# Optimization experiments

Hardware: AMD Instinct MI355X
Metric: run time of the kernel (lower is better)

The kernel has to match this reference:

```python
import jax, jax.numpy as jnp
import numpy as np

NUM_ROUTING_ITERATIONS = 3


def _squash(t, axis=-1):
    # scale * t / ||t||, scale = ||t||^2 / (1 + ||t||^2)
    squared_norm = jnp.sum(t * t, axis=axis, keepdims=True)
    return squared_norm / (1.0 + squared_norm) * t / jnp.sqrt(squared_norm)


def setup_inputs() -> dict:
    key = jax.random.key(0)
    k_x, k_w = jax.random.split(key)
    B, R, C, O, I = 64, 2048, 16, 32, 16
    x = jax.random.normal(k_x, (B, R, I), dtype=jnp.float32)
    W = jax.random.normal(k_w, (R, C, O, I), dtype=jnp.float32)
    return {"x": x, "W": W}


def reference(x, W):
    # u_hat[b,r,c,o] = sum_i W[r,c,o,i] * x[b,r,i]
    u_hat = jnp.einsum('rcoi,bri->brco', W, x)  # [B,R,C,O]
    B, R, C, O = u_hat.shape
    b = jnp.zeros((B, R, C), dtype=u_hat.dtype)  # routing logits
    v = None
    for _ in range(NUM_ROUTING_ITERATIONS):
        c = jax.nn.softmax(b, axis=2)                      # softmax over capsules (dim=2)
        s = jnp.einsum('brc,brco->bro', c, u_hat)          # (c * u_hat).sum(dim=2)
        v = _squash(s, axis=-1)                            # [B,R,O]
        b = b + jnp.einsum('brco,bro->brc', u_hat, v)      # agreement update
    return v
```

## Files before the change

kernel.cpp:

```cpp
#include <hip/hip_runtime.h>

#define R_DIM 2048
#define O_DIM 32
#define I_DIM 16
#define B_DIM 64
#define BB 16

typedef _Float16 half4  __attribute__((ext_vector_type(4)));
typedef float    f32x4  __attribute__((ext_vector_type(4)));

struct SplitH4 { half4 h1, h2; };

__device__ __forceinline__ SplitH4 splitf16x4(const float* __restrict__ p) {
    const float4 f = *(const float4*)p;
    const auto a0 = __builtin_amdgcn_cvt_pkrtz(f.x, f.y);
    const auto a1 = __builtin_amdgcn_cvt_pkrtz(f.z, f.w);
    const auto c0 = __builtin_amdgcn_cvt_pkrtz(f.x - (float)a0[0], f.y - (float)a0[1]);
    const auto c1 = __builtin_amdgcn_cvt_pkrtz(f.z - (float)a1[0], f.w - (float)a1[1]);
    SplitH4 s;
    s.h1[0] = (_Float16)a0[0]; s.h1[1] = (_Float16)a0[1];
    s.h1[2] = (_Float16)a1[0]; s.h1[3] = (_Float16)a1[1];
    s.h2[0] = (_Float16)c0[0]; s.h2[1] = (_Float16)c0[1];
    s.h2[2] = (_Float16)c1[0]; s.h2[3] = (_Float16)c1[1];
    return s;
}

template<int CTRL>
__device__ __forceinline__ float dpp_mv(float v) {
    int t = __builtin_amdgcn_update_dpp(0, __float_as_int(v), CTRL, 0xf, 0xf, true);
    return __int_as_float(t);
}
__device__ __forceinline__ float row16_sum(float v) {
    v += dpp_mv<0xB1>(v);
    v += dpp_mv<0x4E>(v);
    v += dpp_mv<0x124>(v);
    v += dpp_mv<0x128>(v);
    return v;
}
__device__ __forceinline__ float row16_max(float v) {
    v = fmaxf(v, dpp_mv<0xB1>(v));
    v = fmaxf(v, dpp_mv<0x4E>(v));
    v = fmaxf(v, dpp_mv<0x124>(v));
    v = fmaxf(v, dpp_mv<0x128>(v));
    return v;
}
__device__ __forceinline__ float ror1(float v) { return dpp_mv<0x121>(v); }
__device__ __forceinline__ float ror2(float v) { return dpp_mv<0x122>(v); }

__global__ __launch_bounds__(512, 8)
void capsule_routing_kernel(const float* __restrict__ x,
                            const float* __restrict__ W,
                            float* __restrict__ out) {
    __shared__ float u_lds[BB * 512];

    const int tid = threadIdx.x;
    const int bid = blockIdx.x;
    const int r   = ((bid >> 5) << 3) | (bid & 7);
    const int b0  = ((bid >> 3) & 3) * BB;

    {
        const int lane = tid & 63;
        const int w    = tid >> 6;
        const int q    = lane >> 4;
        const int np   = lane & 15;

        const SplitH4 as = splitf16x4(x + ((size_t)(b0 + np) * R_DIM + r) * I_DIM + q * 4);

        const float* Wbase = W + (size_t)r * 8192 + (size_t)(w * 4) * 256 + np * 16 + q * 4;

        const f32x4 zero4 = {0.f, 0.f, 0.f, 0.f};
        #pragma unroll
        for (int t = 0; t < 4; ++t) {
            const int ntile = w * 4 + t;
            const SplitH4 bs = splitf16x4(Wbase + t * 256);

            f32x4 a = __builtin_amdgcn_mfma_f32_16x16x16f16(as.h2, bs.h1, zero4, 0, 0, 0);
            a = __builtin_amdgcn_mfma_f32_16x16x16f16(as.h1, bs.h2, a, 0, 0, 0);
            a = __builtin_amdgcn_mfma_f32_16x16x16f16(as.h1, bs.h1, a, 0, 0, 0);

            const int col = ntile * 16 + np;
            const int v0  = col ^ (q << 3);
            float* pb = u_lds + q * 2048;
            pb[v0]               = a[0];
            pb[512  + (v0 ^ 8)]  = a[1];
            pb[1024 + (v0 ^ 16)] = a[2];
            pb[1536 + (v0 ^ 24)] = a[3];
        }
    }
    __syncthreads();

    if (tid < 256) {
        const int b = tid >> 4;
        const int j = tid & 15;

        const int sw = ((b ^ (b >> 2)) & 3) << 3;
        const float* pb = u_lds + b * 512 + ((2 * j) ^ sw);

        float2 u2p[16];
        {
            int c = j;
            #pragma unroll
            for (int k = 0; k < 16; ++k) {
                u2p[k] = *(const float2*)&pb[c * 32];
                c = (c - 1) & 15;
            }
        }

        float bvv = 0.0f;
        float s0 = 0.f, s1 = 0.f, g = 0.f;

        #pragma unroll
        for (int it = 0; it < 3; ++it) {
            if (it == 0) {
                s0 = 0.f; s1 = 0.f;
                #pragma unroll
                for (int k = 0; k < 16; ++k) { s0 += u2p[k].x; s1 += u2p[k].y; }
                s0 *= 0.0625f; s1 *= 0.0625f;
            } else {
                const float mx = row16_max(bvv);
                const float e  = __expf(bvv - mx);
                const float Z  = row16_sum(e);
                float wA = e * __builtin_amdgcn_rcpf(Z);
                float wB = ror1(wA);
                float sA0 = 0.f, sA1 = 0.f, sB0 = 0.f, sB1 = 0.f;
                #pragma unroll
                for (int m = 0; m < 8; ++m) {
                    if (m) { wA = ror2(wA); wB = ror2(wB); }
                    sA0 = fmaf(wA, u2p[2 * m].x,     sA0);
                    sA1 = fmaf(wA, u2p[2 * m].y,     sA1);
                    sB0 = fmaf(wB, u2p[2 * m + 1].x, sB0);
                    sB1 = fmaf(wB, u2p[2 * m + 1].y, sB1);
                }
                s0 = sA0 + sB0;
                s1 = sA1 + sB1;
            }

            const float nn = row16_sum(fmaf(s0, s0, s1 * s1));
            g = sqrtf(nn) * __builtin_amdgcn_rcpf(1.0f + nn);

            if (it < 2) {
                float accA = 0.f, accB = 0.f;
                #pragma unroll
                for (int m = 0; m < 8; ++m) {
                    if (m) { accA = ror2(accA); accB = ror2(accB); }
                    accA = fmaf(u2p[2 * m].x,     s0, accA);
                    accA = fmaf(u2p[2 * m].y,     s1, accA);
                    accB = fmaf(u2p[2 * m + 1].x, s0, accB);
                    accB = fmaf(u2p[2 * m + 1].y, s1, accB);
                }
                const float acc = ror2(accA) + ror1(accB);
                bvv = fmaf(g, acc, bvv);
            }
        }

        *(float2*)(out + ((size_t)(b0 + b) * R_DIM + r) * O_DIM + 2 * j)
            = make_float2(g * s0, g * s1);
    }
}

extern "C" void kernel_launch(void* const* d_in, const int* in_sizes, int n_in,
                              void* d_out, int out_size, void* d_ws, size_t ws_size,
                              hipStream_t stream) {
    const float* x   = (const float*)d_in[0];
    const float* W   = (const float*)d_in[1];
    float*       out = (float*)d_out;

    dim3 grid(R_DIM * (B_DIM / BB));
    dim3 block(512);
    hipLaunchKernelGGL(capsule_routing_kernel, grid, block, 0, stream, x, W, out);
}
```

Baseline: 120.0 us.

## Process 32 batches per block so every thread runs routing and W is reused more

Doubles the batch tile per block from 16 to 32. Each W tile loaded from global memory now feeds two sets of MFMA products, and the grid shrinks to half as many blocks. All 512 threads take part in the routing phase, where only half did before. The routing reductions are split into four independent accumulator chains rotated by 4 lanes to shorten dependency chains. Cost: LDS use doubles to 64KB per block and the occupancy hint drops to 4 blocks per CU.

```diff
diff --git a/kernel.cpp b/kernel.cpp
--- a/kernel.cpp
+++ b/kernel.cpp
@@ -4,7 +4,7 @@
 #define O_DIM 32
 #define I_DIM 16
 #define B_DIM 64
-#define BB 16
+#define BB 32
 
 typedef _Float16 half4  __attribute__((ext_vector_type(4)));
 typedef float    f32x4  __attribute__((ext_vector_type(4)));
@@ -46,8 +46,10 @@
 }
 __device__ __forceinline__ float ror1(float v) { return dpp_mv<0x121>(v); }
 __device__ __forceinline__ float ror2(float v) { return dpp_mv<0x122>(v); }
+__device__ __forceinline__ float ror3(float v) { return dpp_mv<0x123>(v); }
+__device__ __forceinline__ float ror4(float v) { return dpp_mv<0x124>(v); }
 
-__global__ __launch_bounds__(512, 8)
+__global__ __launch_bounds__(512, 4)
 void capsule_routing_kernel(const float* __restrict__ x,
                             const float* __restrict__ W,
                             float* __restrict__ out) {
@@ -55,8 +57,8 @@
 
     const int tid = threadIdx.x;
     const int bid = blockIdx.x;
-    const int r   = ((bid >> 5) << 3) | (bid & 7);
-    const int b0  = ((bid >> 3) & 3) * BB;
+    const int r   = ((bid >> 4) << 3) | (bid & 7);
+    const int b0  = ((bid >> 3) & 1) * BB;
 
     {
         const int lane = tid & 63;
@@ -64,7 +66,8 @@
         const int q    = lane >> 4;
         const int np   = lane & 15;
 
-        const SplitH4 as = splitf16x4(x + ((size_t)(b0 + np) * R_DIM + r) * I_DIM + q * 4);
+        const SplitH4 as0 = splitf16x4(x + ((size_t)(b0 + np)      * R_DIM + r) * I_DIM + q * 4);
+        const SplitH4 as1 = splitf16x4(x + ((size_t)(b0 + 16 + np) * R_DIM + r) * I_DIM + q * 4);
 
         const float* Wbase = W + (size_t)r * 8192 + (size_t)(w * 4) * 256 + np * 16 + q * 4;
 
@@ -74,35 +77,45 @@
             const int ntile = w * 4 + t;
             const SplitH4 bs = splitf16x4(Wbase + t * 256);
 
-            f32x4 a = __builtin_amdgcn_mfma_f32_16x16x16f16(as.h2, bs.h1, zero4, 0, 0, 0);
-            a = __builtin_amdgcn_mfma_f32_16x16x16f16(as.h1, bs.h2, a, 0, 0, 0);
-            a = __builtin_amdgcn_mfma_f32_16x16x16f16(as.h1, bs.h1, a, 0, 0, 0);
-
             const int col = ntile * 16 + np;
             const int v0  = col ^ (q << 3);
+
+            f32x4 a = __builtin_amdgcn_mfma_f32_16x16x16f16(as0.h2, bs.h1, zero4, 0, 0, 0);
+            a = __builtin_amdgcn_mfma_f32_16x16x16f16(as0.h1, bs.h2, a, 0, 0, 0);
+            a = __builtin_amdgcn_mfma_f32_16x16x16f16(as0.h1, bs.h1, a, 0, 0, 0);
             float* pb = u_lds + q * 2048;
             pb[v0]               = a[0];
             pb[512  + (v0 ^ 8)]  = a[1];
             pb[1024 + (v0 ^ 16)] = a[2];
             pb[1536 + (v0 ^ 24)] = a[3];
+
+            f32x4 c = __builtin_amdgcn_mfma_f32_16x16x16f16(as1.h2, bs.h1, zero4, 0, 0, 0);
+            c = __builtin_amdgcn_mfma_f32_16x16x16f16(as1.h1, bs.h2, c, 0, 0, 0);
+            c = __builtin_amdgcn_mfma_f32_16x16x16f16(as1.h1, bs.h1, c, 0, 0, 0);
+            float* pc = u_lds + 8192 + q * 2048;
+            pc[v0]               = c[0];
+            pc[512  + (v0 ^ 8)]  = c[1];
+            pc[1024 + (v0 ^ 16)] = c[2];
+            pc[1536 + (v0 ^ 24)] = c[3];
         }
     }
     __syncthreads();
 
-    if (tid < 256) {
+    {
         const int b = tid >> 4;
         const int j = tid & 15;
 
-        const int sw = ((b ^ (b >> 2)) & 3) << 3;
-        const float* pb = u_lds + b * 512 + ((2 * j) ^ sw);
+        const int sw  = ((b ^ (b >> 2)) & 3) << 3;
+        const int pxB = (b * 512 + ((2 * j) ^ sw)) * 4;
+        const char* base = (const char*)u_lds;
 
-        float2 u2p[16];
+        float2 X[16];
         {
-            int c = j;
+            int t = j * 128;
             #pragma unroll
             for (int k = 0; k < 16; ++k) {
-                u2p[k] = *(const float2*)&pb[c * 32];
-                c = (c - 1) & 15;
+                X[k] = *(const float2*)(base + ((t & 0x780) | pxB));
+                t -= 128;
             }
         }
 
@@ -112,43 +125,50 @@
         #pragma unroll
         for (int it = 0; it < 3; ++it) {
             if (it == 0) {
-                s0 = 0.f; s1 = 0.f;
-                #pragma unroll
-                for (int k = 0; k < 16; ++k) { s0 += u2p[k].x; s1 += u2p[k].y; }
-                s0 *= 0.0625f; s1 *= 0.0625f;
+                const float e0 = (X[0].x + X[1].x) + (X[2].x  + X[3].x);
+                const float e1 = (X[4].x + X[5].x) + (X[6].x  + X[7].x);
+                const float e2 = (X[8].x + X[9].x) + (X[10].x + X[11].x);
+                const float e3 = (X[12].x + X[13].x) + (X[14].x + X[15].x);
+                const float f0 = (X[0].y + X[1].y) + (X[2].y  + X[3].y);
+                const float f1 = (X[4].y + X[5].y) + (X[6].y  + X[7].y);
+                const float f2 = (X[8].y + X[9].y) + (X[10].y + X[11].y);
+                const float f3 = (X[12].y + X[13].y) + (X[14].y + X[15].y);
+                s0 = ((e0 + e1) + (e2 + e3)) * 0.0625f;
+                s1 = ((f0 + f1) + (f2 + f3)) * 0.0625f;
             } else {
                 const float mx = row16_max(bvv);
                 const float e  = __expf(bvv - mx);
                 const float Z  = row16_sum(e);
-                float wA = e * __builtin_amdgcn_rcpf(Z);
-                float wB = ror1(wA);
+                const float wr = e * __builtin_amdgcn_rcpf(Z);
+                float W0 = wr, W1 = ror1(wr), W2 = ror2(wr), W3 = ror3(wr);
                 float sA0 = 0.f, sA1 = 0.f, sB0 = 0.f, sB1 = 0.f;
+                float sC0 = 0.f, sC1 = 0.f, sD0 = 0.f, sD1 = 0.f;
                 #pragma unroll
-                for (int m = 0; m < 8; ++m) {
-                    if (m) { wA = ror2(wA); wB = ror2(wB); }
-                    sA0 = fmaf(wA, u2p[2 * m].x,     sA0);
-                    sA1 = fmaf(wA, u2p[2 * m].y,     sA1);
-                    sB0 = fmaf(wB, u2p[2 * m + 1].x, sB0);
-                    sB1 = fmaf(wB, u2p[2 * m + 1].y, sB1);
+                for (int m = 0; m < 4; ++m) {
+                    if (m) { W0 = ror4(W0); W1 = ror4(W1); W2 = ror4(W2); W3 = ror4(W3); }
+                    sA0 = fmaf(W0, X[4*m].x,     sA0); sA1 = fmaf(W0, X[4*m].y,     sA1);
+                    sB0 = fmaf(W1, X[4*m + 1].x, sB0); sB1 = fmaf(W1, X[4*m + 1].y, sB1);
+                    sC0 = fmaf(W2, X[4*m + 2].x, sC0); sC1 = fmaf(W2, X[4*m + 2].y, sC1);
+                    sD0 = fmaf(W3, X[4*m + 3].x, sD0); sD1 = fmaf(W3, X[4*m + 3].y, sD1);
                 }
-                s0 = sA0 + sB0;
-                s1 = sA1 + sB1;
+                s0 = (sA0 + sB0) + (sC0 + sD0);
+                s1 = (sA1 + sB1) + (sC1 + sD1);
             }
 
             const float nn = row16_sum(fmaf(s0, s0, s1 * s1));
             g = sqrtf(nn) * __builtin_amdgcn_rcpf(1.0f + nn);
 
             if (it < 2) {
-                float accA = 0.f, accB = 0.f;
+                float aA = 0.f, aB = 0.f, aC = 0.f, aD = 0.f;
                 #pragma unroll
-                for (int m = 0; m < 8; ++m) {
-                    if (m) { accA = ror2(accA); accB = ror2(accB); }
-                    accA = fmaf(u2p[2 * m].x,     s0, accA);
-                    accA = fmaf(u2p[2 * m].y,     s1, accA);
-                    accB = fmaf(u2p[2 * m + 1].x, s0, accB);
-                    accB = fmaf(u2p[2 * m + 1].y, s1, accB);
+                for (int m = 0; m < 4; ++m) {
+                    if (m) { aA = ror4(aA); aB = ror4(aB); aC = ror4(aC); aD = ror4(aD); }
+                    aA = fmaf(X[4*m].x,     s0, aA); aA = fmaf(X[4*m].y,     s1, aA);
+                    aB = fmaf(X[4*m + 1].x, s0, aB); aB = fmaf(X[4*m + 1].y, s1, aB);
+                    aC = fmaf(X[4*m + 2].x, s0, aC); aC = fmaf(X[4*m + 2].y, s1, aC);
+                    aD = fmaf(X[4*m + 3].x, s0, aD); aD = fmaf(X[4*m + 3].y, s1, aD);
                 }
-                const float acc = ror2(accA) + ror1(accB);
+                const float acc = (ror4(aA) + ror3(aB)) + (ror2(aC) + ror1(aD));
                 bvv = fmaf(g, acc, bvv);
             }
         }
```

After: 123.0 us. +2.5%, slower.
